# Kernel optimization log

Measured on AMD Instinct MI355X. Metric: run time of the kernel, lower is better.

Reference implementation:

```python
import jax, jax.numpy as jnp
import numpy as np

IN_SIZE = 512


def setup_inputs() -> dict:
    key = jax.random.key(0)
    k1, k2, k3, k4 = jax.random.split(key, 4)
    B, L, D, O = 8, 256, IN_SIZE, 128
    input1 = jax.random.normal(k1, (B, L, D), dtype=jnp.float32)
    input2 = jax.random.normal(k2, (B, L, D), dtype=jnp.float32)
    w1 = jax.random.normal(k3, (D, O, D), dtype=jnp.float32) * 0.02
    w2 = jax.random.normal(k4, (2 * D + 1, O), dtype=jnp.float32) * 0.02
    return {"input1": input1, "input2": input2, "w1": w1, "w2": w2}


def reference(input1, input2, w1, w2):
    # Bilinear term: [B, Lx, Ly, O]
    logits_1 = jnp.einsum('bxi,ioj,byj->bxyo', input1, w1, input2)
    # Affine term: original tiles+concats [f1; f2; 1] (size 2D+1) then matmuls
    # with w2. Algebraically this is two broadcasted matmuls plus a bias row,
    # avoiding the O(L^2 * 2D) intermediate.
    d = input1.shape[-1]
    w2_a = w2[:d]          # acts on input1 (f1 part)
    w2_b = w2[d:2 * d]     # acts on input2 (f2 part)
    bias = w2[-1]          # the appended ones column
    logits_2 = (jnp.einsum('bxi,io->bxo', input1, w2_a)[:, :, None, :]
                + jnp.einsum('byi,io->byo', input2, w2_b)[:, None, :, :]
                + bias)
    return logits_1 + logits_2
```

## Files before the change

kernel.cpp:

```cpp
#include <hip/hip_runtime.h>
#include <stdint.h>


typedef unsigned short u16;
typedef __attribute__((ext_vector_type(8))) __bf16 bf16x8;
typedef __attribute__((ext_vector_type(4))) float f32x4;

__device__ __forceinline__ u16 f2bf(float f) {
    uint32_t u = __builtin_bit_cast(uint32_t, f);
    u += 0x7fffu + ((u >> 16) & 1u);
    return (u16)(u >> 16);
}

__global__ __launch_bounds__(256) void cvt_kernel(const float* __restrict__ src,
                                                  u16* __restrict__ dst) {
    int i = blockIdx.x * 256 + threadIdx.x;
    float4 v = reinterpret_cast<const float4*>(src)[i];
    uint2 r;
    r.x = (uint32_t)f2bf(v.x) | ((uint32_t)f2bf(v.y) << 16);
    r.y = (uint32_t)f2bf(v.z) | ((uint32_t)f2bf(v.w) << 16);
    reinterpret_cast<uint2*>(dst)[i] = r;
}

__global__ __launch_bounds__(256) void transw_kernel(const float* __restrict__ w1,
                                                     u16* __restrict__ Wt) {
    __shared__ float tile[64][65];
    const int n0 = blockIdx.x * 64;
    const int i0 = blockIdx.y * 64;
    const int t  = threadIdx.x;
    #pragma unroll
    for (int r = 0; r < 16; ++r) {
        int idx = r * 256 + t;
        int li = idx >> 6, ln = idx & 63;
        tile[li][ln] = w1[(size_t)(i0 + li) * 65536 + n0 + ln];
    }
    __syncthreads();
    #pragma unroll
    for (int r = 0; r < 16; ++r) {
        int idx = r * 256 + t;
        int ln = idx >> 6, li = idx & 63;
        Wt[(size_t)(n0 + ln) * 512 + i0 + li] = f2bf(tile[li][ln]);
    }
}

__global__ __launch_bounds__(128) void pk_kernel(const float* __restrict__ in1,
                                                 const float* __restrict__ in2,
                                                 const float* __restrict__ w2,
                                                 float* __restrict__ p1,
                                                 float* __restrict__ p2) {
    const int grp = blockIdx.x;
    const float* src; const float* w; float* dst;
    if (blockIdx.y == 0) { src = in1; w = w2;               dst = p1; }
    else                 { src = in2; w = w2 + 512 * 128;   dst = p2; }
    src += (size_t)grp * 8 * 512;
    dst += (size_t)grp * 8 * 128;
    __shared__ float rows[8][512];
    const int t = threadIdx.x;
    #pragma unroll
    for (int r = 0; r < 32; ++r) {
        int idx = r * 128 + t;
        rows[idx >> 9][idx & 511] = src[idx];
    }
    __syncthreads();
    float acc[8] = {0, 0, 0, 0, 0, 0, 0, 0};
    for (int k = 0; k < 512; ++k) {
        float wv = w[k * 128 + t];
        #pragma unroll
        for (int r = 0; r < 8; ++r) acc[r] += rows[r][k] * wv;
    }
    #pragma unroll
    for (int r = 0; r < 8; ++r) dst[r * 128 + t] = acc[r];
}

__device__ __forceinline__ void gemm_core_128(const u16* __restrict__ A,
                                              const u16* __restrict__ B,
                                              int lda, int ldb,
                                              f32x4 acc[4][4], u16* lds) {
    const int tid  = threadIdx.x;
    const int lane = tid & 63;
    const int w    = tid >> 6;
    const int wm   = w >> 1, wn = w & 1;

    u16* ldsA = lds;
    u16* ldsB = lds + 8192;

    int sm[4], sko[4];
    #pragma unroll
    for (int it = 0; it < 4; ++it) {
        int c  = (w * 4 + it) * 64 + lane;
        int m  = c >> 3;
        sm[it]  = m;
        sko[it] = ((c & 7) ^ (m & 7)) * 8;
    }
    const int fm  = lane & 15;
    const int fkg = lane >> 4;

    for (int k0 = 0; k0 < 512; k0 += 64) {
        __syncthreads();
        #pragma unroll
        for (int it = 0; it < 4; ++it) {
            const u16* ga = A + (size_t)sm[it] * lda + (k0 + sko[it]);
            __builtin_amdgcn_global_load_lds(
                (const __attribute__((address_space(1))) void*)ga,
                (__attribute__((address_space(3))) void*)(ldsA + (w * 4 + it) * 512),
                16, 0, 0);
        }
        #pragma unroll
        for (int it = 0; it < 4; ++it) {
            const u16* gb = B + (size_t)sm[it] * ldb + (k0 + sko[it]);
            __builtin_amdgcn_global_load_lds(
                (const __attribute__((address_space(1))) void*)gb,
                (__attribute__((address_space(3))) void*)(ldsB + (w * 4 + it) * 512),
                16, 0, 0);
        }
        __builtin_amdgcn_s_waitcnt(0);
        __syncthreads();

        #pragma unroll
        for (int ks = 0; ks < 2; ++ks) {
            bf16x8 af[4], bfr[4];
            #pragma unroll
            for (int mt = 0; mt < 4; ++mt) {
                int m  = wm * 64 + mt * 16 + fm;
                int kc = ks * 4 + fkg;
                int ch = m * 8 + (kc ^ (m & 7));
                af[mt] = *reinterpret_cast<const bf16x8*>(ldsA + ch * 8);
            }
            #pragma unroll
            for (int nt = 0; nt < 4; ++nt) {
                int n  = wn * 64 + nt * 16 + fm;
                int kc = ks * 4 + fkg;
                int ch = n * 8 + (kc ^ (n & 7));
                bfr[nt] = *reinterpret_cast<const bf16x8*>(ldsB + ch * 8);
            }
            #pragma unroll
            for (int mt = 0; mt < 4; ++mt)
                #pragma unroll
                for (int nt = 0; nt < 4; ++nt)
                    acc[mt][nt] = __builtin_amdgcn_mfma_f32_16x16x32_bf16(
                        af[mt], bfr[nt], acc[mt][nt], 0, 0, 0);
        }
    }
}

__global__ __launch_bounds__(256) void gemm1_kernel(const u16* __restrict__ Ab,
                                                    const u16* __restrict__ Wt,
                                                    u16* __restrict__ T) {
    __shared__ u16 lds[16384];
    const int    m0 = blockIdx.x * 128;
    const size_t n0 = (size_t)blockIdx.y * 128;
    f32x4 acc[4][4];
    #pragma unroll
    for (int i = 0; i < 4; ++i)
        #pragma unroll
        for (int j = 0; j < 4; ++j) acc[i][j] = f32x4{0.f, 0.f, 0.f, 0.f};
    gemm_core_128(Ab + (size_t)m0 * 512, Wt + n0 * 512, 512, 512, acc, lds);

    const int lane = threadIdx.x & 63;
    const int w = threadIdx.x >> 6;
    const int wm = w >> 1, wn = w & 1;
    const int col = lane & 15, row4 = (lane >> 4) * 4;
    #pragma unroll
    for (int mt = 0; mt < 4; ++mt)
        #pragma unroll
        for (int nt = 0; nt < 4; ++nt) {
            size_t n = n0 + wn * 64 + nt * 16 + col;
            #pragma unroll
            for (int r = 0; r < 4; ++r) {
                int m = m0 + wm * 64 + mt * 16 + row4 + r;
                T[(size_t)m * 65536 + n] = f2bf(acc[mt][nt][r]);
            }
        }
}

__global__ __launch_bounds__(256) void gemm2_kernel(const u16* __restrict__ Tc,
                                                    const u16* __restrict__ B2c,
                                                    const float* __restrict__ p1c,
                                                    const float* __restrict__ p2c,
                                                    const float* __restrict__ bias,
                                                    float* __restrict__ outc) {
    __shared__ u16 lds[16384];
    const int n0 = blockIdx.x * 128;
    const int x  = blockIdx.y;
    const int bb = blockIdx.z;

    const u16* A2 = Tc  + (size_t)bb * 16777216 + (size_t)x * 65536;
    const u16* B2 = B2c + (size_t)bb * 131072  + (size_t)n0 * 512;
    f32x4 acc[4][4];
    #pragma unroll
    for (int i = 0; i < 4; ++i)
        #pragma unroll
        for (int j = 0; j < 4; ++j) acc[i][j] = f32x4{0.f, 0.f, 0.f, 0.f};
    gemm_core_128(A2, B2, 512, 512, acc, lds);

    const float* p1b = p1c + (size_t)bb * 32768 + x * 128;
    const float* p2b = p2c + (size_t)bb * 32768;
    float* outb = outc + (size_t)bb * 8388608 + (size_t)x * 32768;

    const int lane = threadIdx.x & 63;
    const int w = threadIdx.x >> 6;
    const int wm = w >> 1, wn = w & 1;
    const int col = lane & 15, row4 = (lane >> 4) * 4;

    #pragma unroll
    for (int mt = 0; mt < 4; ++mt) {
        const int ob = wm * 64 + mt * 16 + row4;
        const f32x4 pv1 = *reinterpret_cast<const f32x4*>(p1b + ob);
        const f32x4 bv  = *reinterpret_cast<const f32x4*>(bias + ob);
        #pragma unroll
        for (int nt = 0; nt < 4; ++nt) {
            const int y = n0 + wn * 64 + nt * 16 + col;
            const f32x4 pv2 = *reinterpret_cast<const f32x4*>(p2b + (size_t)y * 128 + ob);
            f32x4 v = acc[mt][nt] + pv1 + pv2 + bv;
            *reinterpret_cast<f32x4*>(outb + (size_t)y * 128 + ob) = v;
        }
    }
}

extern "C" void kernel_launch(void* const* d_in, const int* in_sizes, int n_in,
                              void* d_out, int out_size, void* d_ws, size_t ws_size,
                              hipStream_t stream) {
    const float* in1 = (const float*)d_in[0];
    const float* in2 = (const float*)d_in[1];
    const float* w1  = (const float*)d_in[2];
    const float* w2  = (const float*)d_in[3];
    float* out = (float*)d_out;
    char*  ws  = (char*)d_ws;

    u16*   Wt  = (u16*)(ws);
    u16*   Ab  = (u16*)(ws + 67108864);
    u16*   B2b = (u16*)(ws + 69206016);
    float* p1  = (float*)(ws + 71303168);
    float* p2  = (float*)(ws + 72351744);
    u16*   T   = (u16*)(ws + 73400320);

    const size_t base = 73400320ull;
    int C = 1;
    if      (ws_size >= base + 8ull * 33554432ull) C = 8;
    else if (ws_size >= base + 4ull * 33554432ull) C = 4;
    else if (ws_size >= base + 2ull * 33554432ull) C = 2;

    cvt_kernel<<<1024, 256, 0, stream>>>(in1, Ab);
    cvt_kernel<<<1024, 256, 0, stream>>>(in2, B2b);
    transw_kernel<<<dim3(1024, 8), 256, 0, stream>>>(w1, Wt);
    pk_kernel<<<dim3(256, 2), 128, 0, stream>>>(in1, in2, w2, p1, p2);

    for (int b0 = 0; b0 < 8; b0 += C) {
        gemm1_kernel<<<dim3(2 * C, 512), 256, 0, stream>>>(
            Ab + (size_t)b0 * 131072, Wt, T);
        gemm2_kernel<<<dim3(2, 256, C), 256, 0, stream>>>(
            T, B2b + (size_t)b0 * 131072,
            p1 + (size_t)b0 * 32768, p2 + (size_t)b0 * 32768,
            w2 + 131072, out + (size_t)b0 * 8388608);
    }
}
```

Baseline: 800.1 us.

## Stage full-K A tile in LDS, stream B from global, coalesce T stores

Both GEMMs now load a 64-row by full-K (512) A tile into LDS once, then run the whole K loop without per-step barriers. Each wave reads its B fragments straight from global or cache instead of through LDS. gemm1 writes its bf16 output through padded LDS so the stores to T are 16-byte coalesced rows rather than scattered 2-byte writes. Block tiles change to 64x256 and launch bounds now request 2 blocks per CU. The cost is that B fragments are no longer shared through LDS, so each wave does its own global reads, and 64 KB of LDS per block limits occupancy.

```diff
diff --git a/kernel.cpp b/kernel.cpp
--- a/kernel.cpp
+++ b/kernel.cpp
@@ -72,147 +72,127 @@
     for (int r = 0; r < 8; ++r) dst[r * 128 + t] = acc[r];
 }
 
-__device__ __forceinline__ void gemm_core_128(const u16* __restrict__ A,
-                                              const u16* __restrict__ B,
-                                              int lda, int ldb,
-                                              f32x4 acc[4][4], u16* lds) {
-    const int tid  = threadIdx.x;
-    const int lane = tid & 63;
-    const int w    = tid >> 6;
-    const int wm   = w >> 1, wn = w & 1;
-
-    u16* ldsA = lds;
-    u16* ldsB = lds + 8192;
-
-    int sm[4], sko[4];
-    #pragma unroll
-    for (int it = 0; it < 4; ++it) {
-        int c  = (w * 4 + it) * 64 + lane;
-        int m  = c >> 3;
-        sm[it]  = m;
-        sko[it] = ((c & 7) ^ (m & 7)) * 8;
-    }
-    const int fm  = lane & 15;
-    const int fkg = lane >> 4;
-
-    for (int k0 = 0; k0 < 512; k0 += 64) {
-        __syncthreads();
-        #pragma unroll
-        for (int it = 0; it < 4; ++it) {
-            const u16* ga = A + (size_t)sm[it] * lda + (k0 + sko[it]);
-            __builtin_amdgcn_global_load_lds(
-                (const __attribute__((address_space(1))) void*)ga,
-                (__attribute__((address_space(3))) void*)(ldsA + (w * 4 + it) * 512),
-                16, 0, 0);
+__device__ __forceinline__ void stage_rows64(const u16* __restrict__ src, u16* lds) {
+    const int t = threadIdx.x;
+    #pragma unroll
+    for (int it = 0; it < 16; ++it) {
+        int c   = it * 256 + t;
+        int row = c >> 6, p = c & 63;
+        int g   = (p & ~7) | ((p & 7) ^ (row & 7));
+        __builtin_amdgcn_global_load_lds(
+            (const __attribute__((address_space(1))) void*)(src + (size_t)row * 512 + g * 8),
+            (__attribute__((address_space(3))) void*)(lds + (size_t)c * 8),
+            16, 0, 0);
+    }
+    __builtin_amdgcn_s_waitcnt(0);
+    __syncthreads();
+}
+
+__device__ __forceinline__ void kloop(const u16* __restrict__ Bn,
+                                      const u16* lds, f32x4 acc[4][4]) {
+    const int lane = threadIdx.x & 63;
+    const int col = lane & 15, kg = lane >> 4;
+    #pragma unroll 4
+    for (int ks = 0; ks < 16; ++ks) {
+        const int kc = ks * 4 + kg;
+        bf16x8 af[4], bfr[4];
+        #pragma unroll
+        for (int mt = 0; mt < 4; ++mt) {
+            int row = mt * 16 + col;
+            int pos = (kc & ~7) | ((kc & 7) ^ (row & 7));
+            af[mt] = *reinterpret_cast<const bf16x8*>(lds + row * 512 + pos * 8);
         }
         #pragma unroll
-        for (int it = 0; it < 4; ++it) {
-            const u16* gb = B + (size_t)sm[it] * ldb + (k0 + sko[it]);
-            __builtin_amdgcn_global_load_lds(
-                (const __attribute__((address_space(1))) void*)gb,
-                (__attribute__((address_space(3))) void*)(ldsB + (w * 4 + it) * 512),
-                16, 0, 0);
-        }
-        __builtin_amdgcn_s_waitcnt(0);
-        __syncthreads();
-
-        #pragma unroll
-        for (int ks = 0; ks < 2; ++ks) {
-            bf16x8 af[4], bfr[4];
+        for (int nt = 0; nt < 4; ++nt)
+            bfr[nt] = *reinterpret_cast<const bf16x8*>(
+                Bn + (size_t)(nt * 16 + col) * 512 + kc * 8);
+        #pragma unroll
+        for (int mt = 0; mt < 4; ++mt)
             #pragma unroll
-            for (int mt = 0; mt < 4; ++mt) {
-                int m  = wm * 64 + mt * 16 + fm;
-                int kc = ks * 4 + fkg;
-                int ch = m * 8 + (kc ^ (m & 7));
-                af[mt] = *reinterpret_cast<const bf16x8*>(ldsA + ch * 8);
-            }
-            #pragma unroll
-            for (int nt = 0; nt < 4; ++nt) {
-                int n  = wn * 64 + nt * 16 + fm;
-                int kc = ks * 4 + fkg;
-                int ch = n * 8 + (kc ^ (n & 7));
-                bfr[nt] = *reinterpret_cast<const bf16x8*>(ldsB + ch * 8);
-            }
-            #pragma unroll
-            for (int mt = 0; mt < 4; ++mt)
-                #pragma unroll
-                for (int nt = 0; nt < 4; ++nt)
-                    acc[mt][nt] = __builtin_amdgcn_mfma_f32_16x16x32_bf16(
-                        af[mt], bfr[nt], acc[mt][nt], 0, 0, 0);
-        }
-    }
-}
-
-__global__ __launch_bounds__(256) void gemm1_kernel(const u16* __restrict__ Ab,
-                                                    const u16* __restrict__ Wt,
-                                                    u16* __restrict__ T) {
-    __shared__ u16 lds[16384];
-    const int    m0 = blockIdx.x * 128;
-    const size_t n0 = (size_t)blockIdx.y * 128;
+            for (int nt = 0; nt < 4; ++nt)
+                acc[mt][nt] = __builtin_amdgcn_mfma_f32_16x16x32_bf16(
+                    af[mt], bfr[nt], acc[mt][nt], 0, 0, 0);
+    }
+}
+
+__global__ __launch_bounds__(256, 2) void gemm1_kernel(const u16* __restrict__ Ab,
+                                                       const u16* __restrict__ Wt,
+                                                       u16* __restrict__ T) {
+    __shared__ u16 lds[32768];
+    const int m0 = blockIdx.x * 64;
+    const int n0 = blockIdx.y * 256;
+    const int w  = threadIdx.x >> 6;
+    stage_rows64(Ab + (size_t)m0 * 512, lds);
     f32x4 acc[4][4];
     #pragma unroll
     for (int i = 0; i < 4; ++i)
         #pragma unroll
         for (int j = 0; j < 4; ++j) acc[i][j] = f32x4{0.f, 0.f, 0.f, 0.f};
-    gemm_core_128(Ab + (size_t)m0 * 512, Wt + n0 * 512, 512, 512, acc, lds);
-
+    kloop(Wt + ((size_t)n0 + w * 64) * 512, lds, acc);
+
+    __syncthreads();
     const int lane = threadIdx.x & 63;
-    const int w = threadIdx.x >> 6;
-    const int wm = w >> 1, wn = w & 1;
-    const int col = lane & 15, row4 = (lane >> 4) * 4;
+    const int col = lane & 15, kg = lane >> 4;
     #pragma unroll
     for (int mt = 0; mt < 4; ++mt)
         #pragma unroll
         for (int nt = 0; nt < 4; ++nt) {
-            size_t n = n0 + wn * 64 + nt * 16 + col;
+            int n = w * 64 + nt * 16 + col;
             #pragma unroll
             for (int r = 0; r < 4; ++r) {
-                int m = m0 + wm * 64 + mt * 16 + row4 + r;
-                T[(size_t)m * 65536 + n] = f2bf(acc[mt][nt][r]);
+                int m = mt * 16 + kg * 4 + r;
+                lds[m * 264 + n] = f2bf(acc[mt][nt][r]);
             }
         }
-}
-
-__global__ __launch_bounds__(256) void gemm2_kernel(const u16* __restrict__ Tc,
-                                                    const u16* __restrict__ B2c,
-                                                    const float* __restrict__ p1c,
-                                                    const float* __restrict__ p2c,
-                                                    const float* __restrict__ bias,
-                                                    float* __restrict__ outc) {
-    __shared__ u16 lds[16384];
-    const int n0 = blockIdx.x * 128;
-    const int x  = blockIdx.y;
-    const int bb = blockIdx.z;
-
-    const u16* A2 = Tc  + (size_t)bb * 16777216 + (size_t)x * 65536;
-    const u16* B2 = B2c + (size_t)bb * 131072  + (size_t)n0 * 512;
+    __syncthreads();
+    const int t = threadIdx.x;
+    #pragma unroll
+    for (int it = 0; it < 8; ++it) {
+        int c = it * 256 + t;
+        int row = c >> 5, k = c & 31;
+        *reinterpret_cast<uint4*>(T + (size_t)(m0 + row) * 65536 + n0 + k * 8) =
+            *reinterpret_cast<const uint4*>(
+                reinterpret_cast<const char*>(lds) + row * 528 + k * 16);
+    }
+}
+
+__global__ __launch_bounds__(256, 2) void gemm2_kernel(const u16* __restrict__ Tc,
+                                                       const u16* __restrict__ B2c,
+                                                       const float* __restrict__ p1c,
+                                                       const float* __restrict__ p2c,
+                                                       const float* __restrict__ bias,
+                                                       float* __restrict__ outc) {
+    __shared__ u16 lds[32768];
+    const int m0 = blockIdx.x * 64;
+    const int bb = blockIdx.y;
+    const int w  = threadIdx.x >> 6;
+    stage_rows64(Tc + (size_t)bb * 16777216 + (size_t)m0 * 512, lds);
     f32x4 acc[4][4];
     #pragma unroll
     for (int i = 0; i < 4; ++i)
         #pragma unroll
         for (int j = 0; j < 4; ++j) acc[i][j] = f32x4{0.f, 0.f, 0.f, 0.f};
-    gemm_core_128(A2, B2, 512, 512, acc, lds);
-
+    kloop(B2c + (size_t)bb * 131072 + (size_t)(w * 64) * 512, lds, acc);
+
+    const int x   = m0 >> 7;
+    const int ob0 = m0 & 127;
     const float* p1b = p1c + (size_t)bb * 32768 + x * 128;
     const float* p2b = p2c + (size_t)bb * 32768;
     float* outb = outc + (size_t)bb * 8388608 + (size_t)x * 32768;
 
     const int lane = threadIdx.x & 63;
-    const int w = threadIdx.x >> 6;
-    const int wm = w >> 1, wn = w & 1;
-    const int col = lane & 15, row4 = (lane >> 4) * 4;
-
+    const int col = lane & 15, kg = lane >> 4;
     #pragma unroll
     for (int mt = 0; mt < 4; ++mt) {
-        const int ob = wm * 64 + mt * 16 + row4;
-        const f32x4 pv1 = *reinterpret_cast<const f32x4*>(p1b + ob);
-        const f32x4 bv  = *reinterpret_cast<const f32x4*>(bias + ob);
+        const int o = ob0 + mt * 16 + kg * 4;
+        const f32x4 pv1 = *reinterpret_cast<const f32x4*>(p1b + o);
+        const f32x4 bv  = *reinterpret_cast<const f32x4*>(bias + o);
         #pragma unroll
         for (int nt = 0; nt < 4; ++nt) {
-            const int y = n0 + wn * 64 + nt * 16 + col;
-            const f32x4 pv2 = *reinterpret_cast<const f32x4*>(p2b + (size_t)y * 128 + ob);
-            f32x4 v = acc[mt][nt] + pv1 + pv2 + bv;
-            *reinterpret_cast<f32x4*>(outb + (size_t)y * 128 + ob) = v;
+            const int y = w * 64 + nt * 16 + col;
+            const f32x4 pv2 = *reinterpret_cast<const f32x4*>(p2b + (size_t)y * 128 + o);
+            *reinterpret_cast<f32x4*>(outb + (size_t)y * 128 + o) =
+                acc[mt][nt] + pv1 + pv2 + bv;
         }
     }
 }
@@ -246,9 +226,10 @@
     pk_kernel<<<dim3(256, 2), 128, 0, stream>>>(in1, in2, w2, p1, p2);
 
     for (int b0 = 0; b0 < 8; b0 += C) {
-        gemm1_kernel<<<dim3(2 * C, 512), 256, 0, stream>>>(
+        int Cb = (8 - b0 < C) ? (8 - b0) : C;
+        gemm1_kernel<<<dim3(Cb * 4, 256), 256, 0, stream>>>(
             Ab + (size_t)b0 * 131072, Wt, T);
-        gemm2_kernel<<<dim3(2, 256, C), 256, 0, stream>>>(
+        gemm2_kernel<<<dim3(512, Cb), 256, 0, stream>>>(
             T, B2b + (size_t)b0 * 131072,
             p1 + (size_t)b0 * 32768, p2 + (size_t)b0 * 32768,
             w2 + 131072, out + (size_t)b0 * 8388608);
```

Result: slower. 906.5 us (+13.3%).
